# Performance work log

Hardware: AMD Instinct MI355X
Metric: run time of the kernel (lower is better)

## Reference

```python
import jax, jax.numpy as jnp
import numpy as np
from math import factorial, sqrt, pi

MUL = 8
LS = [0, 1, 2]                       # l values for both Rs_in and Rs_out
RS = [(MUL, l) for l in LS]
N_NODES = 20000
N_EDGES = 100000
FEAT = sum(m * (2 * l + 1) for m, l in RS)       # 72
R_TOT = sum(mo * mi * (2 * min(lo, li) + 1) for mo, lo in RS for mi, li in RS)  # 1216
L_MAX = max(LS) + max(LS)            # 4
RSH_DIM = (L_MAX + 1) ** 2           # 25
NB, H = 10, 100                      # radial basis size / hidden width
MIN_R, MAX_R = 0.7, 3.2
SWISH_SCALE = 1.679177               # e3nn rescaled swish factor


def _w3j_entry(j1, j2, j3, m1, m2, m3):
    # complex-basis Wigner 3j (Racah formula)
    if m1 + m2 + m3 != 0 or not (abs(j1 - j2) <= j3 <= j1 + j2):
        return 0.0
    t1, t2 = j2 - m1 - j3, j1 + m2 - j3
    kmin, kmax = max(0, t1, t2), min(j1 + j2 - j3, j1 - m1, j2 + m2)
    s = sum((-1) ** k / (factorial(k) * factorial(k - t1) * factorial(k - t2)
                         * factorial(j1 + j2 - j3 - k) * factorial(j1 - m1 - k) * factorial(j2 + m2 - k))
            for k in range(kmin, kmax + 1))
    pref = (-1) ** (j1 - j2 - m3) * sqrt(
        factorial(j1 + j2 - j3) * factorial(j1 - j2 + j3) * factorial(-j1 + j2 + j3) / factorial(j1 + j2 + j3 + 1)
        * factorial(j1 + m1) * factorial(j1 - m1) * factorial(j2 + m2) * factorial(j2 - m2)
        * factorial(j3 + m3) * factorial(j3 - m3))
    return pref * s


def _real_cob(l):
    # complex->real spherical-harmonic change of basis
    U = np.zeros((2 * l + 1, 2 * l + 1), dtype=complex)
    U[l, l] = 1.0
    s = 1.0 / np.sqrt(2.0)
    for m in range(1, l + 1):
        U[l + m, l + m] = (-1) ** m * s
        U[l + m, l - m] = s
        U[l - m, l - m] = 1j * s
        U[l - m, l + m] = -1j * ((-1) ** m) * s
    return U


def _wigner3j_real(l1, l2, l3):
    w = np.zeros((2 * l1 + 1, 2 * l2 + 1, 2 * l3 + 1))
    for m1 in range(-l1, l1 + 1):
        for m2 in range(-l2, l2 + 1):
            m3 = -m1 - m2
            if abs(m3) <= l3:
                w[m1 + l1, m2 + l2, m3 + l3] = _w3j_entry(l1, l2, l3, m1, m2, m3)
    T = np.einsum('am,bn,cp,mnp->abc', _real_cob(l1), _real_cob(l2), _real_cob(l3), w.astype(complex))
    C = T.real if np.linalg.norm(T.real) >= np.linalg.norm(T.imag) else T.imag
    n = np.linalg.norm(C)
    return (C / n if n > 0 else C).astype(np.float32)


# precomputed constants (coupling coefficients + normalization), as in MinimalNetwork.__init__
C3 = {(lo, li, lf): jnp.asarray(_wigner3j_real(lo, li, lf))
      for _, lo in RS for _, li in RS for lf in range(abs(lo - li), lo + li + 1)}


def _norm_coef():
    nc = np.zeros((len(RS), len(RS)), dtype=np.float32)
    for i, (_, lo) in enumerate(RS):
        num = sum(mi * (2 * min(lo, li) + 1) for mi, li in RS)
        nc[i, :] = sqrt(4 * pi) * sqrt(2 * lo + 1) / sqrt(num)
    return jnp.asarray(nc)

NORM = _norm_coef()


def _swish(x):
    return SWISH_SCALE * x * jax.nn.sigmoid(x)


def _radial(r, Ws):
    # GaussianRadialModel: gaussian basis -> 3 hidden swish layers -> linear out
    centers = jnp.linspace(MIN_R, MAX_R, NB)
    sigma = (MAX_R - MIN_R) / (NB - 1)
    x = jnp.exp(-(((r[:, None] - centers) / sigma) ** 2))
    for W in Ws[:-1]:
        x = _swish(x @ (W / jnp.sqrt(jnp.asarray(W.shape[0], x.dtype))))
    W = Ws[-1]
    return x @ (W / jnp.sqrt(jnp.asarray(W.shape[0], x.dtype)))


def _tensor_message(F_src, rsh, R):
    # F_src: [E, FEAT] gathered source features; rsh: [E, 25]; R: [E, R_TOT]
    E = F_src.shape[0]
    f_offs = np.cumsum([0] + [m * (2 * l + 1) for m, l in RS])
    msgs, r_off = [], 0
    for i, (U, lo) in enumerate(RS):
        acc = jnp.zeros((E, U, 2 * lo + 1), F_src.dtype)
        for j, (V, li) in enumerate(RS):
            nlf = 2 * min(lo, li) + 1
            Rb = R[:, r_off:r_off + U * V * nlf].reshape(E, U, V, nlf)
            r_off += U * V * nlf
            Fb = F_src[:, f_offs[j]:f_offs[j + 1]].reshape(E, V, 2 * li + 1)
            for fi, lf in enumerate(range(abs(lo - li), lo + li + 1)):
                # K[e,mo,mi] = sum_mf C3[mo,mi,mf] * Y_lf[e,mf]
                K = jnp.einsum('oif,ef->eoi', C3[(lo, li, lf)], rsh[:, lf * lf:(lf + 1) * (lf + 1)])
                acc = acc + NORM[i, j] * jnp.einsum('eoi,evi,euv->euo', K, Fb, Rb[..., fi])
        msgs.append(acc.reshape(E, -1))
    return jnp.concatenate(msgs, axis=-1)


def _forward(features, edge_index, radii, rsh, Ws):
    R = _radial(radii, Ws)                                     # [E, R_TOT]
    msg = _tensor_message(features[edge_index[0]], rsh, R)     # [E, FEAT]
    # scatter-add aggregation at target nodes (MessagePassing aggr='add')
    return jnp.zeros((features.shape[0], msg.shape[1]), msg.dtype).at[edge_index[1]].add(msg)


def setup_inputs() -> dict:
    key = jax.random.key(0)
    ks = jax.random.split(key, 8)
    features = jax.random.normal(ks[0], (N_NODES, FEAT), jnp.float32)
    edge_index = jax.random.randint(ks[1], (2, N_EDGES), 0, N_NODES)
    radii = MIN_R + (MAX_R - MIN_R) * jax.random.uniform(ks[2], (N_EDGES,), jnp.float32)
    rsh = jax.random.normal(ks[3], (N_EDGES, RSH_DIM), jnp.float32)
    W0 = jax.random.normal(ks[4], (NB, H), jnp.float32)
    W1 = jax.random.normal(ks[5], (H, H), jnp.float32)
    W2 = jax.random.normal(ks[6], (H, H), jnp.float32)
    W3 = jax.random.normal(ks[7], (H, R_TOT), jnp.float32)
    return {"features": features, "edge_index": edge_index, "radii": radii, "rsh": rsh,
            "W0": W0, "W1": W1, "W2": W2, "W3": W3}


def reference(features, edge_index, radii, rsh, W0, W1, W2, W3):
    return _forward(features, edge_index, radii, rsh, (W0, W1, W2, W3))
```

## Files before the change

### kernel.cpp

```cpp
#include <hip/hip_runtime.h>
#include <hip/hip_bf16.h>
#include <math.h>


#define FEATD 72
#define NCOL 1216
#define SWISH_SCALE 1.679177f

typedef __attribute__((ext_vector_type(8))) short bf16x8;
typedef __attribute__((ext_vector_type(4))) float f32x4;

constexpr int NCOMBO = 19;
constexpr int CB_LO[NCOMBO] = {0,0,0,1,1,1,1,1,1,1,2,2,2,2,2,2,2,2,2};
constexpr int CB_LI[NCOMBO] = {0,1,2,0,1,1,1,2,2,2,0,1,1,1,2,2,2,2,2};
constexpr int CB_LF[NCOMBO] = {0,1,2,1,0,1,2,1,2,3,2,1,2,3,0,1,2,3,4};
constexpr int CB_OFF[NCOMBO] = {0,1,10,35,44,53,80,125,170,245,350,375,420,495,600,625,700,825,1000};
constexpr int CB_SZ[NCOMBO]  = {1,9,25,9,9,27,45,45,75,105,25,45,75,105,25,75,125,175,225};
constexpr int C3TOT = 1225;

constexpr int C3OFFT[3][3][5] = {
  { {0,-1,-1,-1,-1}, {-1,1,-1,-1,-1}, {-1,-1,10,-1,-1} },
  { {-1,35,-1,-1,-1}, {44,53,80,-1,-1}, {-1,125,170,245,-1} },
  { {-1,-1,350,-1,-1}, {-1,375,420,495,-1}, {600,625,700,825,1000} }
};
constexpr int ROFFT[3][3] = {{0,64,128},{192,256,448},{640,704,896}};
constexpr int FOFFT[3]   = {0,8,32};

__device__ const double d_fact[11] = {1.,1.,2.,6.,24.,120.,720.,5040.,40320.,362880.,3628800.};

__device__ double w3j_entry(int j1,int j2,int j3,int m1,int m2,int m3){
  if (m1+m2+m3 != 0) return 0.0;
  int dj = j1-j2; if (dj<0) dj=-dj;
  if (j3 < dj || j3 > j1+j2) return 0.0;
  int t1 = j2 - m1 - j3, t2 = j1 + m2 - j3;
  int kmin = 0; if (t1>kmin) kmin=t1; if (t2>kmin) kmin=t2;
  int kmax = j1+j2-j3; if (j1-m1<kmax) kmax=j1-m1; if (j2+m2<kmax) kmax=j2+m2;
  double s = 0.0;
  for (int k=kmin;k<=kmax;++k){
    double den = d_fact[k]*d_fact[k-t1]*d_fact[k-t2]*d_fact[j1+j2-j3-k]
               * d_fact[j1-m1-k]*d_fact[j2+m2-k];
    s += ((k&1)? -1.0:1.0)/den;
  }
  double pref = sqrt(d_fact[j1+j2-j3]*d_fact[j1-j2+j3]*d_fact[-j1+j2+j3]/d_fact[j1+j2+j3+1]
               * d_fact[j1+m1]*d_fact[j1-m1]*d_fact[j2+m2]*d_fact[j2-m2]
               * d_fact[j3+m3]*d_fact[j3-m3]);
  int ex = j1-j2-m3;
  if (ex & 1) pref = -pref;
  return pref*s;
}

__device__ void cob(int l, int r, int c, double& re, double& im){
  re = 0.0; im = 0.0;
  int mr = r - l, mc = c - l;
  const double s = 0.70710678118654752440;
  if (mr == 0) { if (mc == 0) re = 1.0; return; }
  if (mr > 0) {
    if (mc == mr)       re = (mr & 1) ? -s : s;
    else if (mc == -mr) re = s;
  } else {
    int m = -mr;
    if (mc == -m)      im = s;
    else if (mc == m)  im = (m & 1) ? s : -s;
  }
}

__global__ void c3_combined_kernel(float* __restrict__ C3f){
  __shared__ double sre[225], sim[225];
  const int c = blockIdx.x;
  const int lo = CB_LO[c], li = CB_LI[c], lf = CB_LF[c];
  const int off = CB_OFF[c], sz = CB_SZ[c];
  const int n2 = 2*li+1, n3 = 2*lf+1;
  const int t = threadIdx.x;

  for (int p=t; p<sz; p+=64){
    int a = p/(n2*n3), b = (p/n3)%n2, g = p%n3;
    double re=0.0, im=0.0;
    for (int m1=-lo; m1<=lo; ++m1){
      for (int m2=-li; m2<=li; ++m2){
        int m3 = -m1-m2;
        if (m3 < -lf || m3 > lf) continue;
        double w = w3j_entry(lo,li,lf,m1,m2,m3);
        if (w == 0.0) continue;
        double r1,i1,r2,i2,r3,i3;
        cob(lo, a, m1+lo, r1,i1);
        cob(li, b, m2+li, r2,i2);
        cob(lf, g, m3+lf, r3,i3);
        double rr = r1*r2 - i1*i2, ri = r1*i2 + i1*r2;
        double fr = rr*r3 - ri*i3, fi = rr*i3 + ri*r3;
        re += fr*w; im += fi*w;
      }
    }
    sre[p] = re; sim[p] = im;
  }
  __syncthreads();
  double s2r=0.0, s2i=0.0;
  for (int p=t; p<sz; p+=64){ double x=sre[p], y=sim[p]; s2r+=x*x; s2i+=y*y; }
  for (int m=1; m<64; m<<=1){ s2r += __shfl_xor(s2r, m, 64); s2i += __shfl_xor(s2i, m, 64); }
  bool useRe = (s2r >= s2i);
  double n = sqrt(useRe ? s2r : s2i);
  double inv = (n > 0.0) ? 1.0/n : 1.0;
  for (int p=t; p<sz; p+=64){
    double v = useRe ? sre[p] : sim[p];
    C3f[off+p] = (float)(v*inv);
  }
}

__global__ __launch_bounds__(256) void prep_combined_kernel(
    const float* __restrict__ W3, const float* __restrict__ W1,
    const float* __restrict__ W2, __hip_bfloat16* __restrict__ W3t,
    __hip_bfloat16* __restrict__ W1t, __hip_bfloat16* __restrict__ W2t)
{
  int idx = blockIdx.x*256 + threadIdx.x;
  constexpr int NW3 = 19*8192;
  constexpr int HALF = 7*4*64*8;
  if (idx < NW3){
    int j = idx & 7, lane = (idx>>3)&63, kc = (idx>>9)&15, chunk = idx>>13;
    int ks = kc & 3, ct = kc >> 2;
    int r = ct*16 + (lane&15);
    int k = ks*32 + (lane>>4)*8 + j;
    int lo = CB_LO[chunk], li = CB_LI[chunk], lf = CB_LF[chunk];
    int lmin = lo<li ? lo : li;
    int nlf = 2*lmin+1;
    int fi = lf - (lo>li ? lo-li : li-lo);
    int c = ROFFT[lo][li] + r*nlf + fi;
    float v = (k < 100) ? 0.1f*W3[(size_t)k*NCOL + c] : 0.f;
    W3t[idx] = __float2bfloat16(v);
  } else if (idx < NW3 + 2*HALF){
    int r2 = idx - NW3;
    const float* W = (r2 < HALF) ? W1 : W2;
    __hip_bfloat16* Wt = (r2 < HALF) ? W1t : W2t;
    int r = (r2 < HALF) ? r2 : r2 - HALF;
    int j = r & 7, lane = (r>>3)&63, kc = r>>9;
    int ks = kc & 3, ot = kc >> 2;
    int o = ot*16 + (lane&15);
    int k = ks*32 + (lane>>4)*8 + j;
    float v = (o < 100 && k < 100) ? 0.1f*W[k*100+o] : 0.f;
    Wt[r] = __float2bfloat16(v);
  }
}

constexpr int OF_RT  = 0;
constexpr int OF_ACC = 17408;
constexpr int OF_F   = 27648;
constexpr int OF_KV  = 47104;
constexpr int OF_C3  = 53504;
constexpr int OF_SRC = 58404;
constexpr int OF_TGT = 58660;
constexpr int SMEM_SZ = 58916;

constexpr int OF_BAS  = 0;
constexpr int OF_HA   = 2560;
constexpr int OF_HB   = 19968;

__device__ __forceinline__ float swishf(float s){
  return SWISH_SCALE * s / (1.f + __expf(-s));
}

__device__ __forceinline__ void radial_layer_glb(
    const __hip_bfloat16* __restrict__ sIn,
    const __hip_bfloat16* __restrict__ Wt,
    __hip_bfloat16* __restrict__ sOut,
    int lane, int wv, int lr, int lq)
{
  bf16x8 bf[4];
  #pragma unroll
  for (int ks=0; ks<4; ++ks)
    bf[ks] = *(const bf16x8*)&sIn[(wv*16+lr)*136 + ks*32 + lq*8];
  f32x4 acc[7] = {};
  #pragma unroll
  for (int ks=0; ks<4; ++ks)
    #pragma unroll
    for (int ot=0; ot<7; ++ot){
      bf16x8 a = *(const bf16x8*)&Wt[((ot*4+ks)*64 + lane)*8];
      acc[ot] = __builtin_amdgcn_mfma_f32_16x16x32_bf16(a, bf[ks], acc[ot], 0, 0, 0);
    }
  #pragma unroll
  for (int ot=0; ot<7; ++ot){
    __hip_bfloat16 hv[4];
    #pragma unroll
    for (int r=0; r<4; ++r)
      hv[r] = __float2bfloat16(swishf(acc[ot][r]));
    *(short4*)&sOut[(wv*16+lr)*136 + ot*16 + lq*4] = *(short4*)hv;
  }
  {
    int l2 = lq*16 + lr;
    int row = l2 & 15, q = l2 >> 4;
    short4 z = {0,0,0,0};
    *(short4*)&sOut[(wv*16+row)*136 + 112 + q*4] = z;
  }
}

template<int LO,int LI,int LF>
__device__ __forceinline__ void kv_sec(float* kvb, const float* sC3,
                                       const float* __restrict__ rshrow,
                                       int e, int role)
{
  constexpr int NO = 2*LO+1, NI = 2*LI+1, NF = 2*LF+1;
  constexpr int C3B = C3OFFT[LO][LI][LF];
  float y[NF];
  #pragma unroll
  for (int mf=0; mf<NF; ++mf) y[mf] = rshrow[LF*LF + mf];
  for (int it = role; it < NO*NI; it += 4){
    float s = 0.f;
    #pragma unroll
    for (int mf=0; mf<NF; ++mf) s += sC3[C3B + it*NF + mf] * y[mf];
    kvb[e*25 + it] = s;
  }
}

template<int LO,int LI>
__device__ __forceinline__ void consume_sec(
    const float* sRt, const float* sFf, const float* kvb, float* sAcc,
    int e, int role)
{
  constexpr int NO = 2*LO+1, NI = 2*LI+1;
  constexpr int FO = FOFFT[LI];
  float H[2][NI];
  #pragma unroll
  for (int du=0; du<2; ++du)
    #pragma unroll
    for (int mi=0; mi<NI; ++mi) H[du][mi] = 0.f;

  #pragma unroll
  for (int vg=0; vg<2; ++vg){
    float fb[4*NI];
    #pragma unroll
    for (int p=0; p<NI; ++p)
      *(f32x4*)&fb[p*4] = *(const f32x4*)&sFf[e*76 + FO + vg*4*NI + p*4];
    #pragma unroll
    for (int du=0; du<2; ++du){
      const int u = role*2 + du;
      f32x4 rv = *(const f32x4*)&sRt[e*68 + u*8 + vg*4];
      #pragma unroll
      for (int v=0; v<4; ++v)
        #pragma unroll
        for (int mi=0; mi<NI; ++mi)
          H[du][mi] += rv[v] * fb[v*NI + mi];
    }
  }
  const int u0 = role*2, u1 = role*2 + 1;
  const int b0 = e*40 + ((LO==0) ? u0 : (LO==1) ? u0*3 : u0*5);
  const int b1 = e*40 + ((LO==0) ? u1 : (LO==1) ? u1*3 : u1*5);
  #pragma unroll
  for (int o=0; o<NO; ++o){
    float s0 = 0.f, s1 = 0.f;
    #pragma unroll
    for (int mi=0; mi<NI; ++mi){
      float kvv = kvb[e*25 + o*NI + mi];
      s0 += kvv * H[0][mi];
      s1 += kvv * H[1][mi];
    }
    sAcc[b0 + o] += s0;
    sAcc[b1 + o] += s1;
  }
}

__device__ __forceinline__ void mfma_sec_glb(
    const __hip_bfloat16* __restrict__ gW,
    float* sRt, const bf16x8 (&hf)[4],
    int lane, int wv, int lr, int lq)
{
  f32x4 a4[4] = {};
  #pragma unroll
  for (int ks=0; ks<4; ++ks){
    #pragma unroll
    for (int ct=0; ct<4; ++ct){
      bf16x8 a = *(const bf16x8*)&gW[((ct*4+ks)*64 + lane)*8];
      a4[ct] = __builtin_amdgcn_mfma_f32_16x16x32_bf16(a, hf[ks], a4[ct], 0, 0, 0);
    }
  }
  #pragma unroll
  for (int ct=0; ct<4; ++ct)
    *(f32x4*)&sRt[(wv*16 + lr)*68 + ct*16 + lq*4] = a4[ct];
}

template<int J0,int W>
__device__ __forceinline__ void flush_group(float* sAcc, float* __restrict__ out,
                                            const int* sTgt, int eb, int t,
                                            float nrm, int E)
{
  const int lane = t & 63, wv = t >> 6;
  __builtin_amdgcn_wave_barrier();
  for (int p = lane; p < 16*W; p += 64){
    int el = wv*16 + p/W, j = p%W;
    if (eb + el < E)
      atomicAdd(&out[(size_t)sTgt[el]*FEATD + J0 + j], nrm * sAcc[el*40 + j]);
    sAcc[el*40 + j] = 0.f;
  }
  __builtin_amdgcn_wave_barrier();
}

template<int LO,int LI,int LF>
__device__ __forceinline__ void phase(
    int chunk, const __hip_bfloat16* __restrict__ W3t, const bf16x8 (&hf)[4],
    float* sRt, float* sFf, float* sKV, const float* sC3,
    const float* __restrict__ rshrow, float* sAcc, int t)
{
  const int e = t >> 2, role = t & 3;
  const int lane = t & 63, wv = t >> 6;
  const int lr = lane & 15, lq = lane >> 4;

  kv_sec<LO,LI,LF>(sKV, sC3, rshrow, e, role);
  mfma_sec_glb(W3t + (size_t)chunk*8192, sRt, hf, lane, wv, lr, lq);
  __builtin_amdgcn_wave_barrier();
  consume_sec<LO,LI>(sRt, sFf, sKV, sAcc, e, role);
  __builtin_amdgcn_wave_barrier();
}

__global__ __launch_bounds__(256,2) void fused_kernel(
    const float* __restrict__ feats, const int* __restrict__ ei,
    const float* __restrict__ radii, const float* __restrict__ rsh,
    const float* __restrict__ W0,
    const __hip_bfloat16* __restrict__ W1t, const __hip_bfloat16* __restrict__ W2t,
    const __hip_bfloat16* __restrict__ W3t, const float* __restrict__ C3g,
    float* __restrict__ out, int E)
{
  __shared__ __align__(16) char smem[SMEM_SZ];
  float* sRt  = (float*)(smem + OF_RT);
  float* sAcc = (float*)(smem + OF_ACC);
  float* sFf  = (float*)(smem + OF_F);
  float* sKV  = (float*)(smem + OF_KV);
  float* sC3  = (float*)(smem + OF_C3);
  int*   sSrc = (int*)(smem + OF_SRC);
  int*   sTgt = (int*)(smem + OF_TGT);
  float* sbas = (float*)(smem + OF_BAS);
  __hip_bfloat16* hA = (__hip_bfloat16*)(smem + OF_HA);
  __hip_bfloat16* hB = (__hip_bfloat16*)(smem + OF_HB);

  const int t = threadIdx.x;
  const int eb = blockIdx.x*64;
  const int lane = t & 63, wv = t >> 6;
  const int lr = lane & 15, lq = lane >> 4;

  for (int p=t; p<640; p+=256){
    int er = p/10, k = p%10;
    int eg = eb + er;
    float r = (eg < E) ? radii[eg] : 0.f;
    float c = 0.7f + (2.5f/9.0f)*(float)k;
    float d = (r - c) * (9.0f/2.5f);
    sbas[p] = __expf(-d*d);
  }
  __syncthreads();
  for (int p=t; p<6400; p+=256){
    int er = p/100, o = p%100;
    float s = 0.f;
    #pragma unroll
    for (int k=0;k<10;++k) s += sbas[er*10+k]*W0[k*100+o];
    hA[er*136+o] = __float2bfloat16(swishf(s*0.3162277660168379f));
  }
  for (int p=t; p<64*36; p+=256){
    int er = p/36, k = 100 + p%36;
    hA[er*136+k] = __float2bfloat16(0.f);
  }
  __syncthreads();

  radial_layer_glb(hA, W1t, hB, lane, wv, lr, lq);
  __builtin_amdgcn_wave_barrier();
  radial_layer_glb(hB, W2t, hA, lane, wv, lr, lq);
  __builtin_amdgcn_wave_barrier();

  bf16x8 hf[4];
  #pragma unroll
  for (int ks=0; ks<4; ++ks)
    hf[ks] = *(const bf16x8*)&hA[(wv*16+lr)*136 + ks*32 + lq*8];

  __syncthreads();

  for (int p=t; p<2560; p+=256) sAcc[p] = 0.f;
  for (int p=t; p<64; p+=256){
    int e = eb + p;
    sSrc[p] = (e < E) ? ei[e] : 0;
    sTgt[p] = (e < E) ? ei[E + e] : 0;
  }
  for (int p=t; p<C3TOT; p+=256) sC3[p] = C3g[p];
  __syncthreads();
  for (int p=t; p<64*72; p+=256){
    int el = p/72, j = p%72;
    sFf[el*76 + j] = feats[(size_t)sSrc[el]*72 + j];
  }
  __syncthreads();

  int eg = eb + (t >> 2); if (eg > E-1) eg = E-1;
  const float* rshrow = rsh + (size_t)eg*25;

  phase<0,0,0>( 0, W3t, hf, sRt, sFf, sKV, sC3, rshrow, sAcc, t);
  phase<0,1,1>( 1, W3t, hf, sRt, sFf, sKV, sC3, rshrow, sAcc, t);
  phase<0,2,2>( 2, W3t, hf, sRt, sFf, sKV, sC3, rshrow, sAcc, t);
  flush_group<0,8>(sAcc, out, sTgt, eb, t, 0.72360125f, E);

  phase<1,0,1>( 3, W3t, hf, sRt, sFf, sKV, sC3, rshrow, sAcc, t);
  phase<1,1,0>( 4, W3t, hf, sRt, sFf, sKV, sC3, rshrow, sAcc, t);
  phase<1,1,1>( 5, W3t, hf, sRt, sFf, sKV, sC3, rshrow, sAcc, t);
  phase<1,1,2>( 6, W3t, hf, sRt, sFf, sKV, sC3, rshrow, sAcc, t);
  phase<1,2,1>( 7, W3t, hf, sRt, sFf, sKV, sC3, rshrow, sAcc, t);
  phase<1,2,2>( 8, W3t, hf, sRt, sFf, sKV, sC3, rshrow, sAcc, t);
  phase<1,2,3>( 9, W3t, hf, sRt, sFf, sKV, sC3, rshrow, sAcc, t);
  flush_group<8,24>(sAcc, out, sTgt, eb, t, 0.8204867f, E);

  phase<2,0,2>(10, W3t, hf, sRt, sFf, sKV, sC3, rshrow, sAcc, t);
  phase<2,1,1>(11, W3t, hf, sRt, sFf, sKV, sC3, rshrow, sAcc, t);
  phase<2,1,2>(12, W3t, hf, sRt, sFf, sKV, sC3, rshrow, sAcc, t);
  phase<2,1,3>(13, W3t, hf, sRt, sFf, sKV, sC3, rshrow, sAcc, t);
  phase<2,2,0>(14, W3t, hf, sRt, sFf, sKV, sC3, rshrow, sAcc, t);
  phase<2,2,1>(15, W3t, hf, sRt, sFf, sKV, sC3, rshrow, sAcc, t);
  phase<2,2,2>(16, W3t, hf, sRt, sFf, sKV, sC3, rshrow, sAcc, t);
  phase<2,2,3>(17, W3t, hf, sRt, sFf, sKV, sC3, rshrow, sAcc, t);
  phase<2,2,4>(18, W3t, hf, sRt, sFf, sKV, sC3, rshrow, sAcc, t);
  flush_group<32,40>(sAcc, out, sTgt, eb, t, 0.9341652f, E);
}

extern "C" void kernel_launch(void* const* d_in, const int* in_sizes, int n_in,
                              void* d_out, int out_size, void* d_ws, size_t ws_size,
                              hipStream_t stream)
{
  const float* feats = (const float*)d_in[0];
  const int*   ei    = (const int*)d_in[1];
  const float* radii = (const float*)d_in[2];
  const float* rsh   = (const float*)d_in[3];
  const float* W0    = (const float*)d_in[4];
  const float* W1    = (const float*)d_in[5];
  const float* W2    = (const float*)d_in[6];
  const float* W3    = (const float*)d_in[7];
  float* out = (float*)d_out;
  const int E = in_sizes[2];

  const int EPAD = ((E + 63)/64)*64;
  const int NBLK = EPAD/64;

  char* ws = (char*)d_ws;
  size_t off_b = 0;
  float*  C3f = (float*)(ws + off_b);  off_b += 8192;
  __hip_bfloat16* W3t = (__hip_bfloat16*)(ws + off_b); off_b += 335872;
  __hip_bfloat16* W1t = (__hip_bfloat16*)(ws + off_b); off_b += 30720;
  __hip_bfloat16* W2t = (__hip_bfloat16*)(ws + off_b); off_b += 30720;

  hipMemsetAsync(out, 0, (size_t)out_size*sizeof(float), stream);

  c3_combined_kernel<<<dim3(NCOMBO), dim3(64), 0, stream>>>(C3f);
  prep_combined_kernel<<<dim3((19*8192 + 2*14336 + 255)/256), dim3(256), 0, stream>>>(
      W3, W1, W2, W3t, W1t, W2t);

  fused_kernel<<<dim3(NBLK), dim3(256), 0, stream>>>(
      feats, ei, radii, rsh, W0, W1t, W2t, W3t, C3f, out, E);
}
```

Measured before the change: 347.1 us.

## Merge init kernels, read C3 from global, raise fused kernel occupancy

Combines the C3 coefficient kernel and the weight-prep kernel into one launch, so one kernel launch is saved. The fused kernel no longer copies C3 into shared memory and instead reads it from global memory through cache, which shrinks LDS use by about 5KB. Launch bounds are raised from 2 to 3 blocks per CU. The smaller LDS footprint and the new bound are meant to allow more resident blocks. The cost is more global/L1 traffic in kv_sec and possibly tighter register limits that could cause spills.

Measured after the change: 364.4 us. 5.0% more time.

```diff
diff --git a/kernel.cpp b/kernel.cpp
--- a/kernel.cpp
+++ b/kernel.cpp
@@ -64,53 +64,59 @@
   }
 }
 
-__global__ void c3_combined_kernel(float* __restrict__ C3f){
-  __shared__ double sre[225], sim[225];
-  const int c = blockIdx.x;
-  const int lo = CB_LO[c], li = CB_LI[c], lf = CB_LF[c];
-  const int off = CB_OFF[c], sz = CB_SZ[c];
-  const int n2 = 2*li+1, n3 = 2*lf+1;
-  const int t = threadIdx.x;
-
-  for (int p=t; p<sz; p+=64){
-    int a = p/(n2*n3), b = (p/n3)%n2, g = p%n3;
-    double re=0.0, im=0.0;
-    for (int m1=-lo; m1<=lo; ++m1){
-      for (int m2=-li; m2<=li; ++m2){
-        int m3 = -m1-m2;
-        if (m3 < -lf || m3 > lf) continue;
-        double w = w3j_entry(lo,li,lf,m1,m2,m3);
-        if (w == 0.0) continue;
-        double r1,i1,r2,i2,r3,i3;
-        cob(lo, a, m1+lo, r1,i1);
-        cob(li, b, m2+li, r2,i2);
-        cob(lf, g, m3+lf, r3,i3);
-        double rr = r1*r2 - i1*i2, ri = r1*i2 + i1*r2;
-        double fr = rr*r3 - ri*i3, fi = rr*i3 + ri*r3;
-        re += fr*w; im += fi*w;
-      }
-    }
-    sre[p] = re; sim[p] = im;
-  }
-  __syncthreads();
-  double s2r=0.0, s2i=0.0;
-  for (int p=t; p<sz; p+=64){ double x=sre[p], y=sim[p]; s2r+=x*x; s2i+=y*y; }
-  for (int m=1; m<64; m<<=1){ s2r += __shfl_xor(s2r, m, 64); s2i += __shfl_xor(s2i, m, 64); }
-  bool useRe = (s2r >= s2i);
-  double n = sqrt(useRe ? s2r : s2i);
-  double inv = (n > 0.0) ? 1.0/n : 1.0;
-  for (int p=t; p<sz; p+=64){
-    double v = useRe ? sre[p] : sim[p];
-    C3f[off+p] = (float)(v*inv);
-  }
-}
-
-__global__ __launch_bounds__(256) void prep_combined_kernel(
+__global__ __launch_bounds__(256) void init_kernel(
     const float* __restrict__ W3, const float* __restrict__ W1,
     const float* __restrict__ W2, __hip_bfloat16* __restrict__ W3t,
-    __hip_bfloat16* __restrict__ W1t, __hip_bfloat16* __restrict__ W2t)
-{
-  int idx = blockIdx.x*256 + threadIdx.x;
+    __hip_bfloat16* __restrict__ W1t, __hip_bfloat16* __restrict__ W2t,
+    float* __restrict__ C3f)
+{
+  if (blockIdx.x < NCOMBO){
+    __shared__ double sre[225], sim[225];
+    const int c = blockIdx.x;
+    const int lo = CB_LO[c], li = CB_LI[c], lf = CB_LF[c];
+    const int off = CB_OFF[c], sz = CB_SZ[c];
+    const int n2 = 2*li+1, n3 = 2*lf+1;
+    const int t = threadIdx.x;
+
+    if (t < 64){
+      for (int p=t; p<sz; p+=64){
+        int a = p/(n2*n3), b = (p/n3)%n2, g = p%n3;
+        double re=0.0, im=0.0;
+        for (int m1=-lo; m1<=lo; ++m1){
+          for (int m2=-li; m2<=li; ++m2){
+            int m3 = -m1-m2;
+            if (m3 < -lf || m3 > lf) continue;
+            double w = w3j_entry(lo,li,lf,m1,m2,m3);
+            if (w == 0.0) continue;
+            double r1,i1,r2,i2,r3,i3;
+            cob(lo, a, m1+lo, r1,i1);
+            cob(li, b, m2+li, r2,i2);
+            cob(lf, g, m3+lf, r3,i3);
+            double rr = r1*r2 - i1*i2, ri = r1*i2 + i1*r2;
+            double fr = rr*r3 - ri*i3, fi = rr*i3 + ri*r3;
+            re += fr*w; im += fi*w;
+          }
+        }
+        sre[p] = re; sim[p] = im;
+      }
+    }
+    __syncthreads();
+    if (t < 64){
+      double s2r=0.0, s2i=0.0;
+      for (int p=t; p<sz; p+=64){ double x=sre[p], y=sim[p]; s2r+=x*x; s2i+=y*y; }
+      for (int m=1; m<64; m<<=1){ s2r += __shfl_xor(s2r, m, 64); s2i += __shfl_xor(s2i, m, 64); }
+      bool useRe = (s2r >= s2i);
+      double n = sqrt(useRe ? s2r : s2i);
+      double inv = (n > 0.0) ? 1.0/n : 1.0;
+      for (int p=t; p<sz; p+=64){
+        double v = useRe ? sre[p] : sim[p];
+        C3f[off+p] = (float)(v*inv);
+      }
+    }
+    return;
+  }
+
+  int idx = (blockIdx.x - NCOMBO)*256 + threadIdx.x;
   constexpr int NW3 = 19*8192;
   constexpr int HALF = 7*4*64*8;
   if (idx < NW3){
@@ -143,10 +149,9 @@
 constexpr int OF_ACC = 17408;
 constexpr int OF_F   = 27648;
 constexpr int OF_KV  = 47104;
-constexpr int OF_C3  = 53504;
-constexpr int OF_SRC = 58404;
-constexpr int OF_TGT = 58660;
-constexpr int SMEM_SZ = 58916;
+constexpr int OF_SRC = 53504;
+constexpr int OF_TGT = 53760;
+constexpr int SMEM_SZ = 54016;
 
 constexpr int OF_BAS  = 0;
 constexpr int OF_HA   = 2560;
@@ -191,7 +196,7 @@
 }
 
 template<int LO,int LI,int LF>
-__device__ __forceinline__ void kv_sec(float* kvb, const float* sC3,
+__device__ __forceinline__ void kv_sec(float* kvb, const float* __restrict__ C3g,
                                        const float* __restrict__ rshrow,
                                        int e, int role)
 {
@@ -203,7 +208,7 @@
   for (int it = role; it < NO*NI; it += 4){
     float s = 0.f;
     #pragma unroll
-    for (int mf=0; mf<NF; ++mf) s += sC3[C3B + it*NF + mf] * y[mf];
+    for (int mf=0; mf<NF; ++mf) s += C3g[C3B + it*NF + mf] * y[mf];
     kvb[e*25 + it] = s;
   }
 }
@@ -293,21 +298,21 @@
 template<int LO,int LI,int LF>
 __device__ __forceinline__ void phase(
     int chunk, const __hip_bfloat16* __restrict__ W3t, const bf16x8 (&hf)[4],
-    float* sRt, float* sFf, float* sKV, const float* sC3,
+    float* sRt, float* sFf, float* sKV, const float* __restrict__ C3g,
     const float* __restrict__ rshrow, float* sAcc, int t)
 {
   const int e = t >> 2, role = t & 3;
   const int lane = t & 63, wv = t >> 6;
   const int lr = lane & 15, lq = lane >> 4;
 
-  kv_sec<LO,LI,LF>(sKV, sC3, rshrow, e, role);
+  kv_sec<LO,LI,LF>(sKV, C3g, rshrow, e, role);
   mfma_sec_glb(W3t + (size_t)chunk*8192, sRt, hf, lane, wv, lr, lq);
   __builtin_amdgcn_wave_barrier();
   consume_sec<LO,LI>(sRt, sFf, sKV, sAcc, e, role);
   __builtin_amdgcn_wave_barrier();
 }
 
-__global__ __launch_bounds__(256,2) void fused_kernel(
+__global__ __launch_bounds__(256,3) void fused_kernel(
     const float* __restrict__ feats, const int* __restrict__ ei,
     const float* __restrict__ radii, const float* __restrict__ rsh,
     const float* __restrict__ W0,
@@ -320,7 +325,6 @@
   float* sAcc = (float*)(smem + OF_ACC);
   float* sFf  = (float*)(smem + OF_F);
   float* sKV  = (float*)(smem + OF_KV);
-  float* sC3  = (float*)(smem + OF_C3);
   int*   sSrc = (int*)(smem + OF_SRC);
   int*   sTgt = (int*)(smem + OF_TGT);
   float* sbas = (float*)(smem + OF_BAS);
@@ -372,7 +376,6 @@
     sSrc[p] = (e < E) ? ei[e] : 0;
     sTgt[p] = (e < E) ? ei[E + e] : 0;
   }
-  for (int p=t; p<C3TOT; p+=256) sC3[p] = C3g[p];
   __syncthreads();
   for (int p=t; p<64*72; p+=256){
     int el = p/72, j = p%72;
@@ -383,29 +386,29 @@
   int eg = eb + (t >> 2); if (eg > E-1) eg = E-1;
   const float* rshrow = rsh + (size_t)eg*25;
 
-  phase<0,0,0>( 0, W3t, hf, sRt, sFf, sKV, sC3, rshrow, sAcc, t);
-  phase<0,1,1>( 1, W3t, hf, sRt, sFf, sKV, sC3, rshrow, sAcc, t);
-  phase<0,2,2>( 2, W3t, hf, sRt, sFf, sKV, sC3, rshrow, sAcc, t);
+  phase<0,0,0>( 0, W3t, hf, sRt, sFf, sKV, C3g, rshrow, sAcc, t);
+  phase<0,1,1>( 1, W3t, hf, sRt, sFf, sKV, C3g, rshrow, sAcc, t);
+  phase<0,2,2>( 2, W3t, hf, sRt, sFf, sKV, C3g, rshrow, sAcc, t);
   flush_group<0,8>(sAcc, out, sTgt, eb, t, 0.72360125f, E);
 
-  phase<1,0,1>( 3, W3t, hf, sRt, sFf, sKV, sC3, rshrow, sAcc, t);
-  phase<1,1,0>( 4, W3t, hf, sRt, sFf, sKV, sC3, rshrow, sAcc, t);
-  phase<1,1,1>( 5, W3t, hf, sRt, sFf, sKV, sC3, rshrow, sAcc, t);
-  phase<1,1,2>( 6, W3t, hf, sRt, sFf, sKV, sC3, rshrow, sAcc, t);
-  phase<1,2,1>( 7, W3t, hf, sRt, sFf, sKV, sC3, rshrow, sAcc, t);
-  phase<1,2,2>( 8, W3t, hf, sRt, sFf, sKV, sC3, rshrow, sAcc, t);
-  phase<1,2,3>( 9, W3t, hf, sRt, sFf, sKV, sC3, rshrow, sAcc, t);
+  phase<1,0,1>( 3, W3t, hf, sRt, sFf, sKV, C3g, rshrow, sAcc, t);
+  phase<1,1,0>( 4, W3t, hf, sRt, sFf, sKV, C3g, rshrow, sAcc, t);
+  phase<1,1,1>( 5, W3t, hf, sRt, sFf, sKV, C3g, rshrow, sAcc, t);
+  phase<1,1,2>( 6, W3t, hf, sRt, sFf, sKV, C3g, rshrow, sAcc, t);
+  phase<1,2,1>( 7, W3t, hf, sRt, sFf, sKV, C3g, rshrow, sAcc, t);
+  phase<1,2,2>( 8, W3t, hf, sRt, sFf, sKV, C3g, rshrow, sAcc, t);
+  phase<1,2,3>( 9, W3t, hf, sRt, sFf, sKV, C3g, rshrow, sAcc, t);
   flush_group<8,24>(sAcc, out, sTgt, eb, t, 0.8204867f, E);
 
-  phase<2,0,2>(10, W3t, hf, sRt, sFf, sKV, sC3, rshrow, sAcc, t);
-  phase<2,1,1>(11, W3t, hf, sRt, sFf, sKV, sC3, rshrow, sAcc, t);
-  phase<2,1,2>(12, W3t, hf, sRt, sFf, sKV, sC3, rshrow, sAcc, t);
-  phase<2,1,3>(13, W3t, hf, sRt, sFf, sKV, sC3, rshrow, sAcc, t);
-  phase<2,2,0>(14, W3t, hf, sRt, sFf, sKV, sC3, rshrow, sAcc, t);
-  phase<2,2,1>(15, W3t, hf, sRt, sFf, sKV, sC3, rshrow, sAcc, t);
-  phase<2,2,2>(16, W3t, hf, sRt, sFf, sKV, sC3, rshrow, sAcc, t);
-  phase<2,2,3>(17, W3t, hf, sRt, sFf, sKV, sC3, rshrow, sAcc, t);
-  phase<2,2,4>(18, W3t, hf, sRt, sFf, sKV, sC3, rshrow, sAcc, t);
+  phase<2,0,2>(10, W3t, hf, sRt, sFf, sKV, C3g, rshrow, sAcc, t);
+  phase<2,1,1>(11, W3t, hf, sRt, sFf, sKV, C3g, rshrow, sAcc, t);
+  phase<2,1,2>(12, W3t, hf, sRt, sFf, sKV, C3g, rshrow, sAcc, t);
+  phase<2,1,3>(13, W3t, hf, sRt, sFf, sKV, C3g, rshrow, sAcc, t);
+  phase<2,2,0>(14, W3t, hf, sRt, sFf, sKV, C3g, rshrow, sAcc, t);
+  phase<2,2,1>(15, W3t, hf, sRt, sFf, sKV, C3g, rshrow, sAcc, t);
+  phase<2,2,2>(16, W3t, hf, sRt, sFf, sKV, C3g, rshrow, sAcc, t);
+  phase<2,2,3>(17, W3t, hf, sRt, sFf, sKV, C3g, rshrow, sAcc, t);
+  phase<2,2,4>(18, W3t, hf, sRt, sFf, sKV, C3g, rshrow, sAcc, t);
   flush_group<32,40>(sAcc, out, sTgt, eb, t, 0.9341652f, E);
 }
 
@@ -436,9 +439,9 @@
 
   hipMemsetAsync(out, 0, (size_t)out_size*sizeof(float), stream);
 
-  c3_combined_kernel<<<dim3(NCOMBO), dim3(64), 0, stream>>>(C3f);
-  prep_combined_kernel<<<dim3((19*8192 + 2*14336 + 255)/256), dim3(256), 0, stream>>>(
-      W3, W1, W2, W3t, W1t, W2t);
+  constexpr int PREP_BLKS = (19*8192 + 2*14336 + 255)/256;
+  init_kernel<<<dim3(NCOMBO + PREP_BLKS), dim3(256), 0, stream>>>(
+      W3, W1, W2, W3t, W1t, W2t, C3f);
 
   fused_kernel<<<dim3(NBLK), dim3(256), 0, stream>>>(
       feats, ei, radii, rsh, W0, W1t, W2t, W3t, C3f, out, E);
```
